# Optimization experiments

Measured on AMD Instinct MI355X. Metric: run time of the kernel, lower is better.

Reference implementation:

```python
import jax, jax.numpy as jnp
import numpy as np

NMS_THR = 0.7
TOPK = 128      # fixed post-NMS rois per level (static padding for jit)
OUT = 14        # RoIAlign output size
SAMPLES = 2     # samples per bin per dim (fixed approximation of sampling_ratio=-1)
STRIDES = (32.0, 16.0, 8.0)


def get_channel(a):
    # a: [..., 4] boxes as (cx, cy, w, h); FPN level assignment, clamped to [1, 4]
    s = jnp.sqrt(a[..., 2] * a[..., 3])
    return jnp.clip(jnp.floor(3.0 + jnp.log2(s / 224.0)), 1.0, 4.0)


def cxcywh_to_xyxy(b):
    cx, cy, w, h = b[..., 0], b[..., 1], b[..., 2], b[..., 3]
    return jnp.stack([cx - w / 2, cy - h / 2, cx + w / 2, cy + h / 2], axis=-1)


def pairwise_iou(b):
    x1, y1, x2, y2 = b[:, 0], b[:, 1], b[:, 2], b[:, 3]
    area = jnp.maximum(x2 - x1, 0.0) * jnp.maximum(y2 - y1, 0.0)
    ix1 = jnp.maximum(x1[:, None], x1[None, :])
    iy1 = jnp.maximum(y1[:, None], y1[None, :])
    ix2 = jnp.minimum(x2[:, None], x2[None, :])
    iy2 = jnp.minimum(y2[:, None], y2[None, :])
    inter = jnp.maximum(ix2 - ix1, 0.0) * jnp.maximum(iy2 - iy1, 0.0)
    union = area[:, None] + area[None, :] - inter
    return inter / jnp.maximum(union, 1e-9)


def nms_keep(boxes_xyxy, scores, thr):
    # Greedy NMS over masked scores (-inf entries sort last and are excluded later).
    n = scores.shape[0]
    order = jnp.argsort(-scores)
    iou = pairwise_iou(boxes_xyxy[order])  # [N, N]
    idx = jnp.arange(n)

    def body(sup, i):
        keep_i = ~sup[i]
        sup = sup | (keep_i & (iou[i] > thr) & (idx > i))
        return sup, keep_i

    _, keeps_sorted = jax.lax.scan(body, jnp.zeros(n, dtype=bool), idx)
    return jnp.zeros(n, dtype=bool).at[order].set(keeps_sorted)


def roi_align(feat, boxes):
    # feat: [C, H, W]; boxes: [K, 4]. NOTE: the original prepare_boxes feeds
    # (cx, cy, w, h) straight into RoIAlign, which interprets them as
    # (x1, y1, x2, y2) -- replicated faithfully here. spatial_scale = 1.
    C, H, W = feat.shape
    K = boxes.shape[0]
    x1, y1, x2, y2 = boxes[:, 0], boxes[:, 1], boxes[:, 2], boxes[:, 3]
    rw = jnp.maximum(x2 - x1, 1.0)
    rh = jnp.maximum(y2 - y1, 1.0)
    bw = rw / OUT
    bh = rh / OUT
    # fractional bin offsets, [OUT*SAMPLES]
    f = (jnp.arange(OUT, dtype=feat.dtype)[:, None]
         + (jnp.arange(SAMPLES, dtype=feat.dtype)[None, :] + 0.5) / SAMPLES).reshape(-1)
    ys = y1[:, None] + bh[:, None] * f[None, :]  # [K, S]
    xs = x1[:, None] + bw[:, None] * f[None, :]
    Y = ys[:, :, None]  # [K, S, 1]
    X = xs[:, None, :]  # [K, 1, S]
    valid = (Y > -1.0) & (Y < H) & (X > -1.0) & (X < W)  # [K, S, S]
    Yc = jnp.clip(Y, 0.0, H - 1.0)
    Xc = jnp.clip(X, 0.0, W - 1.0)
    y0 = jnp.floor(Yc)
    x0 = jnp.floor(Xc)
    y0i = y0.astype(jnp.int32)
    x0i = x0.astype(jnp.int32)
    y1i = jnp.minimum(y0i + 1, H - 1)
    x1i = jnp.minimum(x0i + 1, W - 1)
    ly = Yc - y0
    lx = Xc - x0
    hy = 1.0 - ly
    hx = 1.0 - lx
    g = lambda yi, xi: feat[:, yi, xi]  # -> [C, K, S, S]
    val = (g(y0i, x0i) * (hy * hx) + g(y0i, x1i) * (hy * lx)
           + g(y1i, x0i) * (ly * hx) + g(y1i, x1i) * (ly * lx))
    val = val * valid.astype(val.dtype)
    val = val.reshape(C, K, OUT, SAMPLES, OUT, SAMPLES).mean(axis=(3, 5))
    return jnp.transpose(val, (1, 0, 2, 3))  # [K, C, OUT, OUT]


def level_extract(feat, boxes, scores, levs, nl):
    # one image, one target FPN level: mask, NMS, fixed top-K select, RoIAlign
    mask = levs == nl
    msc = jnp.where(mask, scores, -jnp.inf)
    xyxy = cxcywh_to_xyxy(boxes)
    keep = nms_keep(jax.lax.stop_gradient(xyxy), jax.lax.stop_gradient(msc), NMS_THR)
    eff = jnp.where(keep & mask, msc, -jnp.inf)
    vals, sel = jax.lax.top_k(jax.lax.stop_gradient(eff), TOPK)
    valid = jnp.isfinite(vals)
    rois = boxes[sel] * valid[:, None].astype(boxes.dtype)
    out = roi_align(feat, rois)
    return out * valid[:, None, None, None].astype(out.dtype)


def _forward(p32, p16, p8, p4, a32, a16, a8, s32, s16, s8):
    anchors = (a32, a16, a8)  # p4 proposals are computed then discarded in the
    # original (grouping loop only runs l in range(3)); p4 features are never
    # RoIAligned either (nl loops 1..3), so p4 only appears as an unused input.
    levs = jnp.concatenate([get_channel(a) for a in anchors], axis=1)      # [B, N]
    boxes = jnp.concatenate([a * s for a, s in zip(anchors, STRIDES)], axis=1)
    scores = jnp.concatenate([s32, s16, s8], axis=1)
    outs = []
    for nl, feat in zip((1.0, 2.0, 3.0), (p32, p16, p8)):
        fn = jax.vmap(lambda f, b, s, l, nl=nl: level_extract(f, b, s, l, nl))
        outs.append(fn(feat, boxes, scores, levs))  # [B, TOPK, C, 14, 14]
    return jnp.concatenate(outs, axis=1)  # [B, 3*TOPK, C, 14, 14]


def setup_inputs():
    key = jax.random.key(0)
    ks = jax.random.split(key, 10)
    B, C = 2, 256
    p32 = jax.random.normal(ks[0], (B, C, 32, 32), jnp.float32)
    p16 = jax.random.normal(ks[1], (B, C, 64, 64), jnp.float32)
    p8 = jax.random.normal(ks[2], (B, C, 128, 128), jnp.float32)
    p4 = jax.random.normal(ks[3], (B, C, 256, 256), jnp.float32)

    def mk_anchors(k, n, hf):
        k1, k2 = jax.random.split(k)
        cxy = jax.random.uniform(k1, (B, n, 2), jnp.float32) * hf
        wh = 16.0 + jax.random.uniform(k2, (B, n, 2), jnp.float32) * 434.0
        return jnp.concatenate([cxy, wh], axis=-1)

    anchors_32 = mk_anchors(ks[4], 512, 32.0)
    anchors_16 = mk_anchors(ks[5], 1024, 64.0)
    anchors_8 = mk_anchors(ks[6], 2048, 128.0)
    scores_32 = jax.random.normal(ks[7], (B, 512), jnp.float32)
    scores_16 = jax.random.normal(ks[8], (B, 1024), jnp.float32)
    scores_8 = jax.random.normal(ks[9], (B, 2048), jnp.float32)
    return dict(p32=p32, p16=p16, p8=p8, p4=p4,
                anchors_32=anchors_32, anchors_16=anchors_16, anchors_8=anchors_8,
                scores_32=scores_32, scores_16=scores_16, scores_8=scores_8)


def reference(p32, p16, p8, p4, anchors_32, anchors_16, anchors_8,
              scores_32, scores_16, scores_8):
    return _forward(p32, p16, p8, p4, anchors_32, anchors_16, anchors_8,
                    scores_32, scores_16, scores_8)
```

## Files before the change

kernel.cpp:

```cpp
#include <hip/hip_runtime.h>
#include <stdint.h>

#define NMS_THR 0.7f
#define TOPK 128
#define NTOT 3584
#define NROW 4096
#define NW 64
#define OUTSZ 14
#define NSAMP 28

typedef unsigned long long u64;
typedef float vf4 __attribute__((ext_vector_type(4)));
typedef float float2u __attribute__((ext_vector_type(2), aligned(4)));

__device__ __forceinline__ void fetch_anchor(
    const float* __restrict__ a32, const float* __restrict__ a16,
    const float* __restrict__ a8,
    const float* __restrict__ s32, const float* __restrict__ s16,
    const float* __restrict__ s8,
    int b, int i, float* A, float* st, float* sc)
{
    const float* P;
    if (i < 512) {
        P = a32 + (b * 512 + i) * 4;  *st = 32.0f; *sc = s32[b * 512 + i];
    } else if (i < 1536) {
        int j = i - 512;
        P = a16 + (b * 1024 + j) * 4; *st = 16.0f; *sc = s16[b * 1024 + j];
    } else {
        int j = i - 1536;
        P = a8 + (b * 2048 + j) * 4;  *st = 8.0f;  *sc = s8[b * 2048 + j];
    }
    A[0] = P[0]; A[1] = P[1]; A[2] = P[2]; A[3] = P[3];
}

__global__ __launch_bounds__(1024) void sortprep_kernel(
    const float* __restrict__ a32, const float* __restrict__ a16,
    const float* __restrict__ a8,
    const float* __restrict__ s32, const float* __restrict__ s16,
    const float* __restrict__ s8,
    float* __restrict__ sbox,
    float* __restrict__ scbox,
    int* __restrict__ mArr)
{
    __shared__ u64 key[NROW];
    __shared__ int mCount;
    int prob = blockIdx.x;
    int b = prob / 3;
    int nl = prob % 3 + 1;
    int tid = threadIdx.x;

    if (tid == 0) mCount = 0;
    __syncthreads();

    for (int i = tid; i < NTOT; i += 1024) {
        float A[4], st, sc;
        fetch_anchor(a32, a16, a8, s32, s16, s8, b, i, A, &st, &sc);
        float s = sqrtf(__fmul_rn(A[2], A[3]));
        float lv = floorf(__fadd_rn(3.0f, log2f(__fdiv_rn(s, 224.0f))));
        lv = fminf(fmaxf(lv, 1.0f), 4.0f);
        if ((int)lv == nl) {
            unsigned u = __float_as_uint(sc);
            u = (u & 0x80000000u) ? ~u : (u | 0x80000000u);
            unsigned d = ~u;
            int pos = atomicAdd(&mCount, 1);
            key[pos] = ((u64)d << 32) | (unsigned)i;
        }
    }
    __syncthreads();
    int m = mCount;
    int P2 = 64;
    while (P2 < m) P2 <<= 1;
    for (int i = m + tid; i < P2; i += 1024) key[i] = ~0ull;
    __syncthreads();

    for (int k = 2; k <= P2; k <<= 1) {
        for (int j = k >> 1; j > 0; j >>= 1) {
            for (int t = tid; t < P2; t += 1024) {
                int ixj = t ^ j;
                if (ixj > t) {
                    u64 a = key[t], bb = key[ixj];
                    bool up = ((t & k) == 0);
                    if ((a > bb) == up) { key[t] = bb; key[ixj] = a; }
                }
            }
            __syncthreads();
        }
    }

    for (int r = tid; r < m; r += 1024) {
        int orig = (int)(key[r] & 0xffffffffu);
        float A[4], st, sc;
        fetch_anchor(a32, a16, a8, s32, s16, s8, b, orig, A, &st, &sc);
        float cx = A[0] * st, cy = A[1] * st, w = A[2] * st, h = A[3] * st;
        float4 cw = make_float4(cx, cy, w, h);
        float4 v;
        v.x = __fsub_rn(cx, 0.5f * w);
        v.y = __fsub_rn(cy, 0.5f * h);
        v.z = __fadd_rn(cx, 0.5f * w);
        v.w = __fadd_rn(cy, 0.5f * h);
        ((float4*)(sbox + (size_t)prob * NROW * 4))[r] = v;
        ((float4*)(scbox + (size_t)prob * NROW * 4))[r] = cw;
    }
    if (tid == 0) mArr[prob] = m;
}

__global__ __launch_bounds__(256) void maskfill_kernel(
    const float* __restrict__ sbox, const int* __restrict__ mArr,
    u64* __restrict__ mask,
    vf4* __restrict__ out, int n4)
{
    int prob = blockIdx.x >> 10;
    int rgrp = blockIdx.x & 1023;
    int wave = threadIdx.x >> 6;
    int lane = threadIdx.x & 63;
    int row = rgrp * 4 + wave;
    int m = mArr[prob];

    if (row < m) {
        const float4* SB = (const float4*)(sbox + (size_t)prob * NROW * 4);
        float4 bi = SB[row];
        float areai = __fmul_rn(fmaxf(__fsub_rn(bi.z, bi.x), 0.0f),
                                fmaxf(__fsub_rn(bi.w, bi.y), 0.0f));
        u64* outm = mask + ((size_t)prob * NROW + row) * NW;
        int cEnd = (m - 1) >> 6;
        for (int c = row >> 6; c <= cEnd; c++) {
            int col = c * 64 + lane;
            bool p = false;
            if (col < m) {
                float4 bj = SB[col];
                float areaj = __fmul_rn(fmaxf(__fsub_rn(bj.z, bj.x), 0.0f),
                                        fmaxf(__fsub_rn(bj.w, bj.y), 0.0f));
                float ix1 = fmaxf(bi.x, bj.x);
                float iy1 = fmaxf(bi.y, bj.y);
                float ix2 = fminf(bi.z, bj.z);
                float iy2 = fminf(bi.w, bj.w);
                float inter = __fmul_rn(fmaxf(__fsub_rn(ix2, ix1), 0.0f),
                                        fmaxf(__fsub_rn(iy2, iy1), 0.0f));
                float uni = __fsub_rn(__fadd_rn(areai, areaj), inter);
                float iou = __fdiv_rn(inter, fmaxf(uni, 1e-9f));
                p = iou > NMS_THR;
            }
            u64 bal = __ballot(p);
            if (lane == 0) outm[c] = bal;
        }
    }

    vf4 z = (vf4)0.0f;
    int stride = gridDim.x * 256;
    for (int i = blockIdx.x * 256 + threadIdx.x; i < n4; i += stride)
        out[i] = z;
}

__global__ __launch_bounds__(64) void scan_kernel(
    const float* __restrict__ scbox, const int* __restrict__ mArr,
    const u64* __restrict__ mask,
    float* __restrict__ rois,
    int* __restrict__ validOut)
{
    __shared__ int selList[TOPK];
    int prob = blockIdx.x;
    int lane = threadIdx.x;
    int m = mArr[prob];
    const u64* M = mask + (size_t)prob * NROW * NW;

    u64 sup;
    if (lane * 64 >= m) sup = ~0ull;
    else if (lane * 64 + 64 > m) sup = ~0ull << (m & 63);
    else sup = 0ull;

    int kept = 0;
    int cur = 0;
    while (kept < TOPK && cur < m) {
        int cw = cur >> 6;
        u64 validm = (lane < cw) ? 0ull : (lane == cw ? (~0ull << (cur & 63)) : ~0ull);
        u64 avail = ~sup & validm;
        u64 bal = __ballot(avail != 0ull);
        if (bal == 0ull) break;
        int fl = __builtin_ctzll(bal);
        int lo = __shfl((int)(unsigned)avail, fl);
        int hi = __shfl((int)(avail >> 32), fl);
        u64 w = ((u64)(unsigned)hi << 32) | (unsigned)lo;
        int j = fl * 64 + __builtin_ctzll(w);

        if (lane == 0) selList[kept] = j;
        kept++;
        if (lane >= (j >> 6)) sup |= M[(size_t)j * NW + lane];
        cur = j + 1;
    }
    __syncthreads();

    for (int k = lane; k < TOPK; k += 64) {
        float4 rv = make_float4(0.0f, 0.0f, 0.0f, 0.0f);
        int vld = 0;
        if (k < kept) {
            rv = ((const float4*)(scbox + (size_t)prob * NROW * 4))[selList[k]];
            vld = 1;
        }
        ((float4*)(rois + ((size_t)prob * TOPK + k) * 4))[0] = rv;
        validOut[prob * TOPK + k] = vld;
    }
}

__global__ __launch_bounds__(256) void roialign_kernel(
    const float* __restrict__ p32, const float* __restrict__ p16,
    const float* __restrict__ p8,
    const float* __restrict__ rois, const int* __restrict__ validIn,
    float* __restrict__ out)
{
    int roiIdx = blockIdx.x;
    int b = roiIdx / 384;
    int slot = roiIdx - b * 384;
    int lvl = slot / TOPK;
    int k = slot - lvl * TOPK;
    int prob = b * 3 + lvl;

    int vld = validIn[prob * TOPK + k];
    if (!vld) return;

    int W;
    const float* feat;
    if (lvl == 0)      { W = 32;  feat = p32; }
    else if (lvl == 1) { W = 64;  feat = p16; }
    else               { W = 128; feat = p8; }
    int HW = W * W;
    const float* F0 = feat + (size_t)b * 256 * HW;
    float* O = out + (size_t)roiIdx * 256 * 196;
    int tid = threadIdx.x;

    __shared__ int sxb[NSAMP], sy0[NSAMP], sy1[NSAMP];
    __shared__ float swx0[NSAMP], swx1[NSAMP], shy[NSAMP], sly[NSAMP];
    __shared__ int sxv[NSAMP], syv[NSAMP];
    __shared__ int oiL[OUTSZ], ojL[OUTSZ];
    __shared__ int nyx[2];

    if (tid < 2 * NSAMP) {
        const float* R = rois + ((size_t)prob * TOPK + k) * 4;
        float x1 = R[0], y1 = R[1], x2 = R[2], y2 = R[3];
        float rw = fmaxf(__fsub_rn(x2, x1), 1.0f);
        float rh = fmaxf(__fsub_rn(y2, y1), 1.0f);
        float bw = __fdiv_rn(rw, 14.0f);
        float bh = __fdiv_rn(rh, 14.0f);
        int axis = tid / NSAMP;
        int s = tid - axis * NSAMP;
        float fi = (float)(s >> 1) + ((s & 1) ? 0.75f : 0.25f);
        float start = axis ? y1 : x1;
        float bsz = axis ? bh : bw;
        float lim = (float)W;
        float X = __fadd_rn(start, __fmul_rn(bsz, fi));
        bool v = (X > -1.0f) && (X < lim);
        float Xc = fminf(fmaxf(X, 0.0f), lim - 1.0f);
        float x0f = floorf(Xc);
        int x0 = (int)x0f;
        float l = __fsub_rn(Xc, x0f);
        float hh = __fsub_rn(1.0f, l);
        float vf = v ? 1.0f : 0.0f;
        if (axis == 0) {
            int base; float w0, w1;
            if (x0 >= W - 1) { base = W - 2; w0 = 0.0f; w1 = vf; }
            else             { base = x0;    w0 = hh * vf; w1 = l * vf; }
            sxb[s] = base; swx0[s] = w0; swx1[s] = w1; sxv[s] = v ? 1 : 0;
        } else {
            sy0[s] = x0; sy1[s] = min(x0 + 1, W - 1);
            shy[s] = hh * vf; sly[s] = l * vf; syv[s] = v ? 1 : 0;
        }
    }
    __syncthreads();

    if (tid == 0) {
        int n = 0;
        for (int oi = 0; oi < OUTSZ; oi++)
            if (syv[2 * oi] | syv[2 * oi + 1]) oiL[n++] = oi;
        nyx[0] = n;
    }
    if (tid == 1) {
        int n = 0;
        for (int oj = 0; oj < OUTSZ; oj++)
            if (sxv[2 * oj] | sxv[2 * oj + 1]) ojL[n++] = oj;
        nyx[1] = n;
    }
    __syncthreads();

    int ny = nyx[0], nx = nyx[1];
    int total = ny * nx;
    if (total == 0) return;

    int w = tid >> 6;
    int lane = tid & 63;

    for (int ci = w; ci < total; ci += 4) {
        int oi = oiL[ci / nx];
        int oj = ojL[ci - (ci / nx) * nx];
        int sA = oi * 2, sB = sA + 1;
        int tA = oj * 2, tB = tA + 1;
        int y0A = sy0[sA], y1A = sy1[sA], y0B = sy0[sB], y1B = sy1[sB];
        float hyA = shy[sA], lyA = sly[sA], hyB = shy[sB], lyB = sly[sB];
        int xA = sxb[tA], xB = sxb[tB];
        float xw0A = swx0[tA], xw1A = swx1[tA];
        float xw0B = swx0[tB], xw1B = swx1[tB];
        int p = oi * 14 + oj;

        for (int it = 0; it < 4; it++) {
            int c = lane + it * 64;
            const float* F = F0 + c * HW;
            const float* rA0 = F + y0A * W;
            const float* rA1 = F + y1A * W;
            const float* rB0 = F + y0B * W;
            const float* rB1 = F + y1B * W;

            float2u a0 = *(const float2u*)(rA0 + xA);
            float2u a1 = *(const float2u*)(rA1 + xA);
            float2u c0 = *(const float2u*)(rA0 + xB);
            float2u c1 = *(const float2u*)(rA1 + xB);
            float2u b0 = *(const float2u*)(rB0 + xA);
            float2u b1 = *(const float2u*)(rB1 + xA);
            float2u d0 = *(const float2u*)(rB0 + xB);
            float2u d1 = *(const float2u*)(rB1 + xB);

            float s00 = hyA * (xw0A * a0.x + xw1A * a0.y) + lyA * (xw0A * a1.x + xw1A * a1.y);
            float s01 = hyA * (xw0B * c0.x + xw1B * c0.y) + lyA * (xw0B * c1.x + xw1B * c1.y);
            float s10 = hyB * (xw0A * b0.x + xw1A * b0.y) + lyB * (xw0A * b1.x + xw1A * b1.y);
            float s11 = hyB * (xw0B * d0.x + xw1B * d0.y) + lyB * (xw0B * d1.x + xw1B * d1.y);
            O[c * 196 + p] = 0.25f * (s00 + s01 + s10 + s11);
        }
    }
}

extern "C" void kernel_launch(void* const* d_in, const int* in_sizes, int n_in,
                              void* d_out, int out_size, void* d_ws, size_t ws_size,
                              hipStream_t stream) {
    const float* p32 = (const float*)d_in[0];
    const float* p16 = (const float*)d_in[1];
    const float* p8  = (const float*)d_in[2];
    const float* a32 = (const float*)d_in[4];
    const float* a16 = (const float*)d_in[5];
    const float* a8  = (const float*)d_in[6];
    const float* s32 = (const float*)d_in[7];
    const float* s16 = (const float*)d_in[8];
    const float* s8  = (const float*)d_in[9];
    float* out = (float*)d_out;

    const size_t offValid = 3072;
    const size_t offMArr  = offValid + 768;
    const size_t offSbox  = offMArr + 8;
    const size_t offScbox = offSbox + (size_t)6 * NROW * 4;
    const size_t offMask  = offScbox + (size_t)6 * NROW * 4;
    const size_t totalFloats = offMask + (size_t)6 * NROW * NW * 2;

    float* base;
    if (ws_size >= totalFloats * 4) {
        base = (float*)d_ws;
    } else {
        base = (float*)d_in[3];
    }
    float* rois  = base;
    int*   valid = (int*)(base + offValid);
    int*   mArr  = (int*)(base + offMArr);
    float* sbox  = base + offSbox;
    float* scbox = base + offScbox;
    u64*   maskb = (u64*)(base + offMask);

    sortprep_kernel<<<6, 1024, 0, stream>>>(a32, a16, a8, s32, s16, s8,
                                            sbox, scbox, mArr);
    maskfill_kernel<<<6 * 1024, 256, 0, stream>>>(sbox, mArr, maskb,
                                                  (vf4*)out, out_size / 4);
    scan_kernel<<<6, 64, 0, stream>>>(scbox, mArr, maskb, rois, valid);
    roialign_kernel<<<768, 256, 0, stream>>>(p32, p16, p8, rois, valid, out);
}
```

Measured before the change: 375.6 us.

## Replace IoU-mask NMS with in-block greedy scan against kept boxes

Drops the full pairwise IoU bitmask kernel and the separate scan kernel. Instead, one wave walks the sorted candidates and tests each against at most 128 kept boxes held in lane registers, stopping once TOPK boxes are kept. This removes the O(m^2) mask computation and its global-memory traffic, and cuts the number of kernel launches. Output zeroing moves into the RoIAlign kernel, with each block clearing its own RoI slice. It also caps candidates at 2048 per level in shared memory, which could drop candidates if a level ever exceeds that, and the scan is serial per candidate within a single wave.

```diff
diff --git a/kernel.cpp b/kernel.cpp
--- a/kernel.cpp
+++ b/kernel.cpp
@@ -4,8 +4,7 @@
 #define NMS_THR 0.7f
 #define TOPK 128
 #define NTOT 3584
-#define NROW 4096
-#define NW 64
+#define CAP 2048
 #define OUTSZ 14
 #define NSAMP 28
 
@@ -30,20 +29,24 @@
         int j = i - 1536;
         P = a8 + (b * 2048 + j) * 4;  *st = 8.0f;  *sc = s8[b * 2048 + j];
     }
-    A[0] = P[0]; A[1] = P[1]; A[2] = P[2]; A[3] = P[3];
+    float4 v = *(const float4*)P;
+    A[0] = v.x; A[1] = v.y; A[2] = v.z; A[3] = v.w;
 }
 
-__global__ __launch_bounds__(1024) void sortprep_kernel(
+__global__ __launch_bounds__(1024) void select_kernel(
     const float* __restrict__ a32, const float* __restrict__ a16,
     const float* __restrict__ a8,
     const float* __restrict__ s32, const float* __restrict__ s16,
     const float* __restrict__ s8,
-    float* __restrict__ sbox,
-    float* __restrict__ scbox,
-    int* __restrict__ mArr)
+    float* __restrict__ rois,
+    int* __restrict__ validOut)
 {
-    __shared__ u64 key[NROW];
-    __shared__ int mCount;
+    __shared__ u64 key[CAP];
+    __shared__ float bx1[CAP], by1[CAP], bx2[CAP], by2[CAP];
+    __shared__ float bar[CAP];
+    __shared__ int selList[TOPK];
+    __shared__ int mCount, keptCount;
+
     int prob = blockIdx.x;
     int b = prob / 3;
     int nl = prob % 3 + 1;
@@ -63,11 +66,12 @@
             u = (u & 0x80000000u) ? ~u : (u | 0x80000000u);
             unsigned d = ~u;
             int pos = atomicAdd(&mCount, 1);
-            key[pos] = ((u64)d << 32) | (unsigned)i;
+            if (pos < CAP) key[pos] = ((u64)d << 32) | (unsigned)i;
         }
     }
     __syncthreads();
     int m = mCount;
+    if (m > CAP) m = CAP;
     int P2 = 64;
     while (P2 < m) P2 <<= 1;
     for (int i = m + tid; i < P2; i += 1024) key[i] = ~0ull;
@@ -92,111 +96,70 @@
         float A[4], st, sc;
         fetch_anchor(a32, a16, a8, s32, s16, s8, b, orig, A, &st, &sc);
         float cx = A[0] * st, cy = A[1] * st, w = A[2] * st, h = A[3] * st;
-        float4 cw = make_float4(cx, cy, w, h);
-        float4 v;
-        v.x = __fsub_rn(cx, 0.5f * w);
-        v.y = __fsub_rn(cy, 0.5f * h);
-        v.z = __fadd_rn(cx, 0.5f * w);
-        v.w = __fadd_rn(cy, 0.5f * h);
-        ((float4*)(sbox + (size_t)prob * NROW * 4))[r] = v;
-        ((float4*)(scbox + (size_t)prob * NROW * 4))[r] = cw;
-    }
-    if (tid == 0) mArr[prob] = m;
-}
-
-__global__ __launch_bounds__(256) void maskfill_kernel(
-    const float* __restrict__ sbox, const int* __restrict__ mArr,
-    u64* __restrict__ mask,
-    vf4* __restrict__ out, int n4)
-{
-    int prob = blockIdx.x >> 10;
-    int rgrp = blockIdx.x & 1023;
-    int wave = threadIdx.x >> 6;
-    int lane = threadIdx.x & 63;
-    int row = rgrp * 4 + wave;
-    int m = mArr[prob];
-
-    if (row < m) {
-        const float4* SB = (const float4*)(sbox + (size_t)prob * NROW * 4);
-        float4 bi = SB[row];
-        float areai = __fmul_rn(fmaxf(__fsub_rn(bi.z, bi.x), 0.0f),
-                                fmaxf(__fsub_rn(bi.w, bi.y), 0.0f));
-        u64* outm = mask + ((size_t)prob * NROW + row) * NW;
-        int cEnd = (m - 1) >> 6;
-        for (int c = row >> 6; c <= cEnd; c++) {
-            int col = c * 64 + lane;
-            bool p = false;
-            if (col < m) {
-                float4 bj = SB[col];
-                float areaj = __fmul_rn(fmaxf(__fsub_rn(bj.z, bj.x), 0.0f),
-                                        fmaxf(__fsub_rn(bj.w, bj.y), 0.0f));
-                float ix1 = fmaxf(bi.x, bj.x);
-                float iy1 = fmaxf(bi.y, bj.y);
-                float ix2 = fminf(bi.z, bj.z);
-                float iy2 = fminf(bi.w, bj.w);
-                float inter = __fmul_rn(fmaxf(__fsub_rn(ix2, ix1), 0.0f),
-                                        fmaxf(__fsub_rn(iy2, iy1), 0.0f));
-                float uni = __fsub_rn(__fadd_rn(areai, areaj), inter);
-                float iou = __fdiv_rn(inter, fmaxf(uni, 1e-9f));
-                p = iou > NMS_THR;
+        float x1 = __fsub_rn(cx, 0.5f * w);
+        float y1 = __fsub_rn(cy, 0.5f * h);
+        float x2 = __fadd_rn(cx, 0.5f * w);
+        float y2 = __fadd_rn(cy, 0.5f * h);
+        bx1[r] = x1; by1[r] = y1; bx2[r] = x2; by2[r] = y2;
+        bar[r] = __fmul_rn(fmaxf(__fsub_rn(x2, x1), 0.0f),
+                           fmaxf(__fsub_rn(y2, y1), 0.0f));
+    }
+    __syncthreads();
+
+    if (tid < 64) {
+        int lane = tid;
+        float ax1 = 0, ay1 = 0, ax2 = 0, ay2 = 0, aa = 0;
+        float px1 = 0, py1 = 0, px2 = 0, py2 = 0, pa = 0;
+        int kept = 0;
+        float nx1 = 0, ny1 = 0, nx2 = 0, ny2 = 0, na = 0;
+        if (m > 0) { nx1 = bx1[0]; ny1 = by1[0]; nx2 = bx2[0]; ny2 = by2[0]; na = bar[0]; }
+        for (int j = 0; j < m; ++j) {
+            float cx1 = nx1, cy1 = ny1, cx2 = nx2, cy2 = ny2, ca = na;
+            int jn = (j + 1 < m) ? j + 1 : j;
+            nx1 = bx1[jn]; ny1 = by1[jn]; nx2 = bx2[jn]; ny2 = by2[jn]; na = bar[jn];
+
+            float i1 = fmaxf(ax1, cx1), i2 = fmaxf(ay1, cy1);
+            float i3 = fminf(ax2, cx2), i4 = fminf(ay2, cy2);
+            float inA = __fmul_rn(fmaxf(__fsub_rn(i3, i1), 0.0f),
+                                  fmaxf(__fsub_rn(i4, i2), 0.0f));
+            float unA = __fsub_rn(__fadd_rn(aa, ca), inA);
+            bool sup = __fdiv_rn(inA, fmaxf(unA, 1e-9f)) > NMS_THR;
+
+            i1 = fmaxf(px1, cx1); i2 = fmaxf(py1, cy1);
+            i3 = fminf(px2, cx2); i4 = fminf(py2, cy2);
+            float inB = __fmul_rn(fmaxf(__fsub_rn(i3, i1), 0.0f),
+                                  fmaxf(__fsub_rn(i4, i2), 0.0f));
+            float unB = __fsub_rn(__fadd_rn(pa, ca), inB);
+            sup = sup || (__fdiv_rn(inB, fmaxf(unB, 1e-9f)) > NMS_THR);
+
+            u64 bal = __ballot(sup);
+            if (bal == 0ull) {
+                if (kept < 64) {
+                    if (lane == kept) { ax1 = cx1; ay1 = cy1; ax2 = cx2; ay2 = cy2; aa = ca; }
+                } else {
+                    if (lane == kept - 64) { px1 = cx1; py1 = cy1; px2 = cx2; py2 = cy2; pa = ca; }
+                }
+                if (lane == 0) selList[kept] = j;
+                kept++;
+                if (kept >= TOPK) break;
             }
-            u64 bal = __ballot(p);
-            if (lane == 0) outm[c] = bal;
-        }
-    }
-
-    vf4 z = (vf4)0.0f;
-    int stride = gridDim.x * 256;
-    for (int i = blockIdx.x * 256 + threadIdx.x; i < n4; i += stride)
-        out[i] = z;
-}
-
-__global__ __launch_bounds__(64) void scan_kernel(
-    const float* __restrict__ scbox, const int* __restrict__ mArr,
-    const u64* __restrict__ mask,
-    float* __restrict__ rois,
-    int* __restrict__ validOut)
-{
-    __shared__ int selList[TOPK];
-    int prob = blockIdx.x;
-    int lane = threadIdx.x;
-    int m = mArr[prob];
-    const u64* M = mask + (size_t)prob * NROW * NW;
-
-    u64 sup;
-    if (lane * 64 >= m) sup = ~0ull;
-    else if (lane * 64 + 64 > m) sup = ~0ull << (m & 63);
-    else sup = 0ull;
-
-    int kept = 0;
-    int cur = 0;
-    while (kept < TOPK && cur < m) {
-        int cw = cur >> 6;
-        u64 validm = (lane < cw) ? 0ull : (lane == cw ? (~0ull << (cur & 63)) : ~0ull);
-        u64 avail = ~sup & validm;
-        u64 bal = __ballot(avail != 0ull);
-        if (bal == 0ull) break;
-        int fl = __builtin_ctzll(bal);
-        int lo = __shfl((int)(unsigned)avail, fl);
-        int hi = __shfl((int)(avail >> 32), fl);
-        u64 w = ((u64)(unsigned)hi << 32) | (unsigned)lo;
-        int j = fl * 64 + __builtin_ctzll(w);
-
-        if (lane == 0) selList[kept] = j;
-        kept++;
-        if (lane >= (j >> 6)) sup |= M[(size_t)j * NW + lane];
-        cur = j + 1;
-    }
-    __syncthreads();
-
-    for (int k = lane; k < TOPK; k += 64) {
+        }
+        if (lane == 0) keptCount = kept;
+    }
+    __syncthreads();
+
+    int kept = keptCount;
+    for (int k = tid; k < TOPK; k += 1024) {
         float4 rv = make_float4(0.0f, 0.0f, 0.0f, 0.0f);
         int vld = 0;
         if (k < kept) {
-            rv = ((const float4*)(scbox + (size_t)prob * NROW * 4))[selList[k]];
+            int orig = (int)(key[selList[k]] & 0xffffffffu);
+            float A[4], st, sc;
+            fetch_anchor(a32, a16, a8, s32, s16, s8, b, orig, A, &st, &sc);
+            rv = make_float4(A[0] * st, A[1] * st, A[2] * st, A[3] * st);
             vld = 1;
         }
-        ((float4*)(rois + ((size_t)prob * TOPK + k) * 4))[0] = rv;
+        ((float4*)rois)[prob * TOPK + k] = rv;
         validOut[prob * TOPK + k] = vld;
     }
 }
@@ -213,6 +176,13 @@
     int lvl = slot / TOPK;
     int k = slot - lvl * TOPK;
     int prob = b * 3 + lvl;
+    int tid = threadIdx.x;
+
+    float* O = out + (size_t)roiIdx * 256 * 196;
+
+    vf4 z = (vf4)0.0f;
+    vf4* O4 = (vf4*)O;
+    for (int i = tid; i < 12544; i += 256) O4[i] = z;
 
     int vld = validIn[prob * TOPK + k];
     if (!vld) return;
@@ -224,8 +194,6 @@
     else               { W = 128; feat = p8; }
     int HW = W * W;
     const float* F0 = feat + (size_t)b * 256 * HW;
-    float* O = out + (size_t)roiIdx * 256 * 196;
-    int tid = threadIdx.x;
 
     __shared__ int sxb[NSAMP], sy0[NSAMP], sy1[NSAMP];
     __shared__ float swx0[NSAMP], swx1[NSAMP], shy[NSAMP], sly[NSAMP];
@@ -339,12 +307,7 @@
     const float* s8  = (const float*)d_in[9];
     float* out = (float*)d_out;
 
-    const size_t offValid = 3072;
-    const size_t offMArr  = offValid + 768;
-    const size_t offSbox  = offMArr + 8;
-    const size_t offScbox = offSbox + (size_t)6 * NROW * 4;
-    const size_t offMask  = offScbox + (size_t)6 * NROW * 4;
-    const size_t totalFloats = offMask + (size_t)6 * NROW * NW * 2;
+    const size_t totalFloats = 3072 + 768;
 
     float* base;
     if (ws_size >= totalFloats * 4) {
@@ -353,16 +316,9 @@
         base = (float*)d_in[3];
     }
     float* rois  = base;
-    int*   valid = (int*)(base + offValid);
-    int*   mArr  = (int*)(base + offMArr);
-    float* sbox  = base + offSbox;
-    float* scbox = base + offScbox;
-    u64*   maskb = (u64*)(base + offMask);
-
-    sortprep_kernel<<<6, 1024, 0, stream>>>(a32, a16, a8, s32, s16, s8,
-                                            sbox, scbox, mArr);
-    maskfill_kernel<<<6 * 1024, 256, 0, stream>>>(sbox, mArr, maskb,
-                                                  (vf4*)out, out_size / 4);
-    scan_kernel<<<6, 64, 0, stream>>>(scbox, mArr, maskb, rois, valid);
+    int*   valid = (int*)(base + 3072);
+
+    select_kernel<<<6, 1024, 0, stream>>>(a32, a16, a8, s32, s16, s8,
+                                          rois, valid);
     roialign_kernel<<<768, 256, 0, stream>>>(p32, p16, p8, rois, valid, out);
 }
```

Result: slower. 624.1 us (+66.2%).
